# Performance work log

Measured on AMD Instinct MI355X. Metric: run time of the kernel, lower is better.

Reference implementation:

```python
import jax, jax.numpy as jnp
import numpy as np

A, B, I, H, O = 400, 64, 50, 192, 3   # num_agents, batch, input_dim, hidden_dim, output_dim
ADIM, NH = 128, 8                      # attention_dim, num_heads
HD = ADIM // NH
SCALE = HD ** -0.5
EPS = 1e-5


def _ln(x, g, b):
    mu = jnp.mean(x, -1, keepdims=True)
    v = jnp.mean((x - mu) ** 2, -1, keepdims=True)
    return (x - mu) * jax.lax.rsqrt(v + EPS) * g + b


def setup_inputs() -> dict:
    key = jax.random.key(0)
    ks = jax.random.split(key, 12)
    s = 0.05
    n = lambda k, shape: (jax.random.normal(k, shape, jnp.float32) * s)
    return {
        'x': jax.random.normal(ks[0], (B, I), jnp.float32),
        'ln_in_g': jnp.ones((A, I), jnp.float32), 'ln_in_b': jnp.zeros((A, I), jnp.float32),
        'W1': n(ks[1], (A, I, H)), 'b1': jnp.zeros((A, H), jnp.float32),
        'Ws1': n(ks[2], (A, I, H)), 'bs1': jnp.zeros((A, H), jnp.float32),
        'W2': n(ks[3], (A, H, H)), 'b2': jnp.zeros((A, H), jnp.float32),
        'Ws2': n(ks[4], (A, H, H)), 'bs2': jnp.zeros((A, H), jnp.float32),
        'W3': n(ks[5], (A, H, H)), 'b3': jnp.zeros((A, H), jnp.float32),
        'ln_h_g': jnp.ones((A, H), jnp.float32), 'ln_h_b': jnp.zeros((A, H), jnp.float32),
        'Wout': n(ks[6], (A, H, O)), 'bout': jnp.zeros((A, O), jnp.float32),
        'aln_g': jnp.ones((H,), jnp.float32), 'aln_b': jnp.zeros((H,), jnp.float32),
        'Wq': n(ks[7], (H, ADIM)), 'bq': jnp.zeros((ADIM,), jnp.float32),
        'Wk': n(ks[8], (H, ADIM)), 'bk': jnp.zeros((ADIM,), jnp.float32),
        'Wv': n(ks[9], (H, ADIM)), 'bv': jnp.zeros((ADIM,), jnp.float32),
        'Wo': n(ks[10], (ADIM, H)), 'bo': jnp.zeros((H,), jnp.float32),
    }


def _forward(x, ln_in_g, ln_in_b, W1, b1, Ws1, bs1, W2, b2, Ws2, bs2, W3, b3,
             ln_h_g, ln_h_b, Wout, bout, aln_g, aln_b, Wq, bq, Wk, bk, Wv, bv, Wo, bo):
    gelu = lambda t: jax.nn.gelu(t, approximate=False)  # torch F.gelu default = exact erf
    # per-agent input LayerNorm (shared stats, per-agent affine) -> [A, B, I]
    xn = _ln(x[None, :, :], ln_in_g[:, None, :], ln_in_b[:, None, :])
    # agent MLPs as batched GEMMs over agent axis
    h1 = gelu(jnp.einsum('abi,aih->abh', xn, W1) + b1[:, None, :]) \
         + jnp.einsum('abi,aih->abh', xn, Ws1) + bs1[:, None, :]
    h2 = gelu(jnp.einsum('abh,ahk->abk', h1, W2) + b2[:, None, :]) \
         + jnp.einsum('abh,ahk->abk', h1, Ws2) + bs2[:, None, :]
    h3 = _ln(h2 + jnp.einsum('abh,ahk->abk', h2, W3) + b3[:, None, :],
             ln_h_g[:, None, :], ln_h_b[:, None, :])  # [A, B, H]
    # cross-SREK attention across the agent axis
    y = _ln(h3, aln_g, aln_b)
    q = (y @ Wq + bq).reshape(A, B, NH, HD).transpose(1, 2, 0, 3)  # [B, NH, A, HD]
    k = (y @ Wk + bk).reshape(A, B, NH, HD).transpose(1, 2, 0, 3)
    v = (y @ Wv + bv).reshape(A, B, NH, HD).transpose(1, 2, 0, 3)
    attn = jax.nn.softmax(jnp.einsum('bhad,bhcd->bhac', q, k) * SCALE, axis=-1)
    o = jnp.einsum('bhac,bhcd->bhad', attn, v).transpose(2, 0, 1, 3).reshape(A, B, ADIM)
    attended = h3 + (o @ Wo + bo)  # residual (dropout off in eval)
    # per-agent output heads -> [A, B, O]
    logits = jnp.einsum('abh,aho->abo', attended, Wout) + bout[:, None, :]
    return logits


def reference(x, ln_in_g, ln_in_b, W1, b1, Ws1, bs1, W2, b2, Ws2, bs2, W3, b3,
              ln_h_g, ln_h_b, Wout, bout, aln_g, aln_b, Wq, bq, Wk, bk, Wv, bv, Wo, bo):
    return _forward(x, ln_in_g, ln_in_b, W1, b1, Ws1, bs1, W2, b2, Ws2, bs2, W3, b3,
                    ln_h_g, ln_h_b, Wout, bout, aln_g, aln_b, Wq, bq, Wk, bk, Wv, bv, Wo, bo)
```

## Files before the change

### kernel.cpp

```cpp
#include <hip/hip_runtime.h>
#include <math.h>

#define AGENTS 400
#define BATCH  64
#define IDIM   50
#define HDIM   192
#define ODIM   3
#define ADIMM  128
#define NHEADS 8
#define HEADD  16
#define LN_EPS 1e-5f

#define PA   200
#define PAM  192
#define POUT 136

typedef __bf16 bf16x8 __attribute__((ext_vector_type(8)));
typedef float  f32x4  __attribute__((ext_vector_type(4)));

__device__ __forceinline__ float gelu_exact(float x) {
    return 0.5f * x * (1.0f + erff(x * 0.70710678118654752f));
}

__device__ __forceinline__ unsigned pack_bf16x2(float a, float b) {
    unsigned short ua = __builtin_bit_cast(unsigned short, (__bf16)a);
    unsigned short ub = __builtin_bit_cast(unsigned short, (__bf16)b);
    return (unsigned)ua | ((unsigned)ub << 16);
}

__device__ __forceinline__ int as_swz(int row, int col) {
    return ((((col >> 3) ^ (row & 7)) << 3) | (col & 7));
}
__device__ __forceinline__ void st_as(__bf16* As_, int row, int col, float v) {
    As_[row * PAM + as_swz(row, col)] = (__bf16)v;
}
__device__ __forceinline__ float ld_as(const __bf16* As_, int row, int col) {
    return (float)As_[row * PAM + as_swz(row, col)];
}
__device__ __forceinline__ bf16x8 ld_afrag(const __bf16* As_, int row, int k0) {
    int blk = (((k0 >> 3) ^ (row & 7)) << 3);
    return *(const bf16x8*)&As_[row * PAM + blk];
}

#define VMWAIT0()   do { asm volatile("s_waitcnt vmcnt(0)" ::: "memory"); \
                         __builtin_amdgcn_sched_barrier(0); } while (0)
#define BARRIER()   do { __builtin_amdgcn_s_barrier(); \
                         __builtin_amdgcn_sched_barrier(0); } while (0)

struct WPtrs { const float *W1, *Ws1, *W2, *Ws2, *W3; };

__device__ __forceinline__ void issue_slot(int s, float* buf0, float* buf1,
                                           const WPtrs& P, const int* kloc,
                                           const int* nsw, int tid)
{
    const float* M; int c, kdm1;
    if (s < 4)       { M = (s & 1) ? P.Ws1 : P.W1; c = s >> 1;      kdm1 = IDIM - 1; }
    else if (s < 16) { int u = s - 4; M = (u & 1) ? P.Ws2 : P.W2; c = u >> 1; kdm1 = HDIM - 1; }
    else             { M = P.W3; c = s - 16; kdm1 = HDIM - 1; }
    float* dst = (s & 1) ? buf1 : buf0;
    #pragma unroll
    for (int i = 0; i < 6; i++) {
        int kg = c * 32 + kloc[i];
        kg = (kg <= kdm1) ? kg : kdm1;
        const float* src = M + (size_t)kg * HDIM + nsw[i];
        __builtin_amdgcn_global_load_lds(
            (const __attribute__((address_space(1))) void*)src,
            (__attribute__((address_space(3))) void*)(dst + (i * 256 + tid) * 4),
            16, 0, 0);
    }
    __builtin_amdgcn_sched_barrier(0);
}

__device__ __forceinline__ void slot_mfma_f32(f32x4 (&acc)[4][3], const __bf16* As_,
                                              const float* Wbuf, int c, int n0, int lane)
{
    const int r = lane & 15, g = lane >> 4;
    bf16x8 bf[3];
    #pragma unroll
    for (int t = 0; t < 3; t++) {
        int cs = (n0 + 16 * t + r) ^ (g << 3);
        #pragma unroll
        for (int j = 0; j < 8; j++)
            bf[t][j] = (__bf16)Wbuf[(g * 8 + j) * HDIM + cs];
    }
    #pragma unroll
    for (int rg = 0; rg < 4; rg++) {
        bf16x8 af = ld_afrag(As_, 16 * rg + r, c * 32 + g * 8);
        #pragma unroll
        for (int t = 0; t < 3; t++)
            acc[rg][t] = __builtin_amdgcn_mfma_f32_16x16x32_bf16(af, bf[t], acc[rg][t], 0, 0, 0);
    }
}

__global__ __launch_bounds__(256, 2) void mlp_kernel(
    const float* __restrict__ x,
    const float* __restrict__ ln_in_g, const float* __restrict__ ln_in_b,
    const float* __restrict__ W1, const float* __restrict__ b1,
    const float* __restrict__ Ws1, const float* __restrict__ bs1,
    const float* __restrict__ W2, const float* __restrict__ b2,
    const float* __restrict__ Ws2, const float* __restrict__ bs2,
    const float* __restrict__ W3, const float* __restrict__ b3,
    const float* __restrict__ ln_h_g, const float* __restrict__ ln_h_b,
    const float* __restrict__ aln_g, const float* __restrict__ aln_b,
    const float* __restrict__ Wq, const float* __restrict__ bq,
    const float* __restrict__ Wk, const float* __restrict__ bk,
    const float* __restrict__ Wv, const float* __restrict__ bv,
    float* __restrict__ h3out,
    float* __restrict__ qT, float* __restrict__ kT, float* __restrict__ vT)
{
    const int a    = blockIdx.x;
    const int tid  = threadIdx.x;
    const int wave = tid >> 6, lane = tid & 63;
    const int r = lane & 15, g = lane >> 4;
    const int n0 = 48 * wave;

    __shared__ __align__(16) __bf16 As[64 * PAM];
    __shared__ __align__(16) float  Wbuf[2][32 * HDIM];
    __shared__ float mu_s[64], rs_s[64];

    int kloc[6], nsw[6];
    #pragma unroll
    for (int i = 0; i < 6; i++) {
        int w = i * 1024 + tid * 4;
        kloc[i] = w / HDIM;
        int np = w - kloc[i] * HDIM;
        nsw[i] = np ^ (((kloc[i] >> 3) & 3) << 3);
    }

    const WPtrs P = {
        W1  + (size_t)a * IDIM * HDIM,
        Ws1 + (size_t)a * IDIM * HDIM,
        W2  + (size_t)a * HDIM * HDIM,
        Ws2 + (size_t)a * HDIM * HDIM,
        W3  + (size_t)a * HDIM * HDIM };

    {
        int rr = tid >> 2, l = tid & 3;
        float s = 0.f, ss = 0.f;
        for (int k = l; k < IDIM; k += 4) { float v = x[rr * IDIM + k]; s += v; ss += v * v; }
        s  += __shfl_down(s, 2, 4);  s  += __shfl_down(s, 1, 4);
        ss += __shfl_down(ss, 2, 4); ss += __shfl_down(ss, 1, 4);
        if (l == 0) {
            float mu = s * (1.0f / IDIM);
            float var = ss * (1.0f / IDIM) - mu * mu;
            mu_s[rr] = mu;
            rs_s[rr] = rsqrtf(var + LN_EPS);
        }
    }
    __syncthreads();

    issue_slot(0, Wbuf[0], Wbuf[1], P, kloc, nsw, tid);

    for (int sidx = tid; sidx < 64 * 64; sidx += 256) {
        int rr = sidx >> 6, k = sidx & 63;
        float v = 0.f;
        if (k < IDIM)
            v = (x[rr * IDIM + k] - mu_s[rr]) * rs_s[rr] * ln_in_g[a * IDIM + k] + ln_in_b[a * IDIM + k];
        st_as(As, rr, k, v);
    }
    __syncthreads();

    {
        f32x4 acc1[4][3], acc2[4][3];
        #pragma unroll
        for (int i = 0; i < 4; i++)
            #pragma unroll
            for (int t = 0; t < 3; t++) { acc1[i][t] = (f32x4)0.f; acc2[i][t] = (f32x4)0.f; }
        #pragma unroll
        for (int s = 0; s < 4; s++) {
            if (s < 3) issue_slot(s + 1, Wbuf[0], Wbuf[1], P, kloc, nsw, tid);
            if ((s & 1) == 0) slot_mfma_f32(acc1, As, Wbuf[s & 1], s >> 1, n0, lane);
            else              slot_mfma_f32(acc2, As, Wbuf[s & 1], s >> 1, n0, lane);
            VMWAIT0();
            BARRIER();
        }
        issue_slot(4, Wbuf[0], Wbuf[1], P, kloc, nsw, tid);
        #pragma unroll
        for (int t = 0; t < 3; t++) {
            int col = n0 + 16 * t + r;
            float bb  = b1[a * HDIM + col];
            float bbs = bs1[a * HDIM + col];
            #pragma unroll
            for (int rg = 0; rg < 4; rg++)
                #pragma unroll
                for (int i = 0; i < 4; i++) {
                    int row = 16 * rg + 4 * g + i;
                    st_as(As, row, col, gelu_exact(acc1[rg][t][i] + bb) + acc2[rg][t][i] + bbs);
                }
        }
        __syncthreads();
    }

    {
        f32x4 acc1[4][3], acc2[4][3];
        #pragma unroll
        for (int i = 0; i < 4; i++)
            #pragma unroll
            for (int t = 0; t < 3; t++) { acc1[i][t] = (f32x4)0.f; acc2[i][t] = (f32x4)0.f; }
        #pragma unroll
        for (int s = 4; s < 16; s++) {
            if (s < 15) issue_slot(s + 1, Wbuf[0], Wbuf[1], P, kloc, nsw, tid);
            if ((s & 1) == 0) slot_mfma_f32(acc1, As, Wbuf[s & 1], (s - 4) >> 1, n0, lane);
            else              slot_mfma_f32(acc2, As, Wbuf[s & 1], (s - 4) >> 1, n0, lane);
            VMWAIT0();
            BARRIER();
        }
        issue_slot(16, Wbuf[0], Wbuf[1], P, kloc, nsw, tid);
        #pragma unroll
        for (int t = 0; t < 3; t++) {
            int col = n0 + 16 * t + r;
            float bb  = b2[a * HDIM + col];
            float bbs = bs2[a * HDIM + col];
            #pragma unroll
            for (int rg = 0; rg < 4; rg++)
                #pragma unroll
                for (int i = 0; i < 4; i++) {
                    int row = 16 * rg + 4 * g + i;
                    st_as(As, row, col, gelu_exact(acc1[rg][t][i] + bb) + acc2[rg][t][i] + bbs);
                }
        }
        __syncthreads();
    }

    {
        f32x4 acc[4][3];
        #pragma unroll
        for (int i = 0; i < 4; i++)
            #pragma unroll
            for (int t = 0; t < 3; t++) acc[i][t] = (f32x4)0.f;
        #pragma unroll
        for (int s = 16; s < 22; s++) {
            if (s < 21) issue_slot(s + 1, Wbuf[0], Wbuf[1], P, kloc, nsw, tid);
            slot_mfma_f32(acc, As, Wbuf[s & 1], s - 16, n0, lane);
            VMWAIT0();
            BARRIER();
        }
        #pragma unroll
        for (int t = 0; t < 3; t++) {
            int col = n0 + 16 * t + r;
            float bb = b3[a * HDIM + col];
            #pragma unroll
            for (int rg = 0; rg < 4; rg++)
                #pragma unroll
                for (int i = 0; i < 4; i++) {
                    int row = 16 * rg + 4 * g + i;
                    st_as(As, row, col, ld_as(As, row, col) + acc[rg][t][i] + bb);
                }
        }
        __syncthreads();
    }

    {
        int rr = tid >> 2, l = tid & 3;
        float s = 0.f, ss = 0.f;
        for (int k = l; k < HDIM; k += 4) { float v = ld_as(As, rr, k); s += v; ss += v * v; }
        s  += __shfl_down(s, 2, 4);  s  += __shfl_down(s, 1, 4);
        ss += __shfl_down(ss, 2, 4); ss += __shfl_down(ss, 1, 4);
        if (l == 0) {
            float mu = s * (1.0f / HDIM);
            float var = ss * (1.0f / HDIM) - mu * mu;
            mu_s[rr] = mu;
            rs_s[rr] = rsqrtf(var + LN_EPS);
        }
    }
    __syncthreads();
    for (int sidx = tid; sidx < 64 * 48; sidx += 256) {
        int rr = sidx / 48, q = sidx - rr * 48;
        int c = q * 4;
        __bf16* p = &As[rr * PAM + as_swz(rr, c)];
        float4 gv = *(const float4*)&ln_h_g[a * HDIM + c];
        float4 bv = *(const float4*)&ln_h_b[a * HDIM + c];
        float mu = mu_s[rr], rs = rs_s[rr];
        float4 o;
        o.x = ((float)p[0] - mu) * rs * gv.x + bv.x;
        o.y = ((float)p[1] - mu) * rs * gv.y + bv.y;
        o.z = ((float)p[2] - mu) * rs * gv.z + bv.z;
        o.w = ((float)p[3] - mu) * rs * gv.w + bv.w;
        *(float4*)&h3out[((size_t)a * BATCH + rr) * HDIM + c] = o;
        p[0] = (__bf16)o.x; p[1] = (__bf16)o.y; p[2] = (__bf16)o.z; p[3] = (__bf16)o.w;
    }
    __syncthreads();

    {
        int rr = tid >> 2, l = tid & 3;
        float s = 0.f, ss = 0.f;
        for (int k = l; k < HDIM; k += 4) { float v = ld_as(As, rr, k); s += v; ss += v * v; }
        s  += __shfl_down(s, 2, 4);  s  += __shfl_down(s, 1, 4);
        ss += __shfl_down(ss, 2, 4); ss += __shfl_down(ss, 1, 4);
        if (l == 0) {
            float mu = s * (1.0f / HDIM);
            float var = ss * (1.0f / HDIM) - mu * mu;
            mu_s[rr] = mu;
            rs_s[rr] = rsqrtf(var + LN_EPS);
        }
    }
    __syncthreads();
    for (int sidx = tid; sidx < 64 * HDIM; sidx += 256) {
        int rr = sidx / HDIM, c = sidx - rr * HDIM;
        float v = (ld_as(As, rr, c) - mu_s[rr]) * rs_s[rr] * aln_g[c] + aln_b[c];
        st_as(As, rr, c, v);
    }
    __syncthreads();

    #pragma unroll
    for (int p = 0; p < 2; p++) {
        const int nb = 192 * p + 48 * wave;
        const float* wA[3];
        #pragma unroll
        for (int t = 0; t < 3; t++) {
            int nt = nb + 16 * t;
            const float* base = (nt < 128) ? Wq : (nt < 256) ? Wk : Wv;
            wA[t] = base + (nt & 127);
        }
        f32x4 acc[4][3];
        #pragma unroll
        for (int i = 0; i < 4; i++)
            #pragma unroll
            for (int t = 0; t < 3; t++) acc[i][t] = (f32x4)0.f;

        float buf[2][24];
        #pragma unroll
        for (int t = 0; t < 3; t++)
            #pragma unroll
            for (int j = 0; j < 8; j++)
                buf[0][t * 8 + j] = wA[t][(g * 8 + j) * ADIMM + r];
        #pragma unroll
        for (int c = 0; c < 6; c++) {
            const int cur = c & 1, nxt = cur ^ 1;
            if (c < 5) {
                #pragma unroll
                for (int t = 0; t < 3; t++)
                    #pragma unroll
                    for (int j = 0; j < 8; j++)
                        buf[nxt][t * 8 + j] = wA[t][((c + 1) * 32 + g * 8 + j) * ADIMM + r];
            }
            bf16x8 bfr[3];
            #pragma unroll
            for (int t = 0; t < 3; t++)
                #pragma unroll
                for (int j = 0; j < 8; j++)
                    bfr[t][j] = (__bf16)buf[cur][t * 8 + j];
            #pragma unroll
            for (int rg = 0; rg < 4; rg++) {
                bf16x8 af = ld_afrag(As, 16 * rg + r, c * 32 + g * 8);
                #pragma unroll
                for (int t = 0; t < 3; t++)
                    acc[rg][t] = __builtin_amdgcn_mfma_f32_16x16x32_bf16(af, bfr[t], acc[rg][t], 0, 0, 0);
            }
        }

        #pragma unroll
        for (int t = 0; t < 3; t++) {
            int n = nb + 16 * t + r;
            int which = n >> 7, cc = n & 127, hh = cc >> 4, dd = cc & 15;
            const float* bp = (which == 0) ? bq : (which == 1) ? bk : bv;
            float* op = (which == 0) ? qT : (which == 1) ? kT : vT;
            float bb = bp[cc];
            #pragma unroll
            for (int rg = 0; rg < 4; rg++)
                #pragma unroll
                for (int i = 0; i < 4; i++) {
                    int brow = 16 * rg + 4 * g + i;
                    op[(((size_t)brow * NHEADS + hh) * AGENTS + a) * HEADD + dd] = acc[rg][t][i] + bb;
                }
        }
    }
}

template<int NC, int KD, int NT, int NRG, int LDW, int PITCH>
__device__ __forceinline__ void gemm_bpass(f32x4 (&acc)[NRG][NT],
                                           const float* const* wptr,
                                           const __bf16* Asrc, int lane)
{
    const int r = lane & 15, g = lane >> 4;
    float buf[2][NT * 8];

    #pragma unroll
    for (int t = 0; t < NT; t++)
        #pragma unroll
        for (int j = 0; j < 8; j++) {
            int k = g * 8 + j;
            buf[0][t * 8 + j] = (k < KD) ? wptr[t][k * LDW + r] : 0.f;
        }

    #pragma unroll
    for (int c = 0; c < NC; c++) {
        const int cur = c & 1, nxt = cur ^ 1;
        if (c + 1 < NC) {
            #pragma unroll
            for (int t = 0; t < NT; t++)
                #pragma unroll
                for (int j = 0; j < 8; j++) {
                    int k = (c + 1) * 32 + g * 8 + j;
                    buf[nxt][t * 8 + j] = (k < KD) ? wptr[t][k * LDW + r] : 0.f;
                }
        }
        bf16x8 bfr[NT];
        #pragma unroll
        for (int t = 0; t < NT; t++)
            #pragma unroll
            for (int j = 0; j < 8; j++)
                bfr[t][j] = (__bf16)buf[cur][t * 8 + j];
        #pragma unroll
        for (int rg = 0; rg < NRG; rg++) {
            bf16x8 af = *(const bf16x8*)&Asrc[(16 * rg + r) * PITCH + c * 32 + g * 8];
            #pragma unroll
            for (int t = 0; t < NT; t++)
                acc[rg][t] = __builtin_amdgcn_mfma_f32_16x16x32_bf16(af, bfr[t], acc[rg][t], 0, 0, 0);
        }
    }
}

#define PKA 24
#define PVA 408
#define PPA 232

__global__ __launch_bounds__(256, 2) void attn_kernel(
    const float* __restrict__ qT, const float* __restrict__ kT,
    const float* __restrict__ vT, float* __restrict__ oT)
{
    const int bh   = blockIdx.x;
    const int b    = bh >> 3, h = bh & 7;
    const int tid  = threadIdx.x;
    const int wave = tid >> 6, lane = tid & 63;
    const int r = lane & 15, g = lane >> 4;

    __shared__ __align__(16) __bf16 Ks[AGENTS * PKA];
    __shared__ __align__(16) __bf16 Vt[16 * PVA];
    __shared__ __align__(16) __bf16 Ps[4][16 * PPA];

    const float* kp = kT + (size_t)bh * AGENTS * HEADD;
    const float* vp = vT + (size_t)bh * AGENTS * HEADD;
    for (int idx4 = tid; idx4 < AGENTS * HEADD / 4; idx4 += 256) {
        int a_ = idx4 >> 2, d0 = (idx4 & 3) << 2;
        float4 kv = *(const float4*)(kp + a_ * HEADD + d0);
        float4 vv = *(const float4*)(vp + a_ * HEADD + d0);
        *(uint2*)&Ks[a_ * PKA + d0] =
            make_uint2(pack_bf16x2(kv.x, kv.y), pack_bf16x2(kv.z, kv.w));
        Vt[(d0 + 0) * PVA + a_] = (__bf16)vv.x;
        Vt[(d0 + 1) * PVA + a_] = (__bf16)vv.y;
        Vt[(d0 + 2) * PVA + a_] = (__bf16)vv.z;
        Vt[(d0 + 3) * PVA + a_] = (__bf16)vv.w;
    }
    __bf16* Pw = Ps[wave];
    for (int z = lane; z < 16 * 16; z += 64)
        Pw[(z >> 4) * PPA + 208 + (z & 15)] = (__bf16)0.f;
    __syncthreads();

    float qf[8];
    auto loadq = [&](int mt_) {
        if (g < 2) {
            const float* qp = qT + ((size_t)bh * AGENTS + mt_ * 16 + r) * HEADD + g * 8;
            float4 v0 = *(const float4*)qp;
            float4 v1 = *(const float4*)(qp + 4);
            qf[0] = v0.x; qf[1] = v0.y; qf[2] = v0.z; qf[3] = v0.w;
            qf[4] = v1.x; qf[5] = v1.y; qf[6] = v1.z; qf[7] = v1.w;
        }
    };
    loadq(wave);

    for (int mt = wave; mt < 25; mt += 4) {
        const int m0 = mt * 16;

        bf16x8 aq;
        #pragma unroll
        for (int j = 0; j < 8; j++)
            aq[j] = (g < 2) ? (__bf16)(qf[j] * 0.25f) : (__bf16)0.f;

        f32x4 sacc[25];
        #pragma unroll
        for (int t = 0; t < 25; t++) {
            bf16x8 bk_ = *(const bf16x8*)&Ks[(t * 16 + r) * PKA + (g & 1) * 8];
            sacc[t] = __builtin_amdgcn_mfma_f32_16x16x32_bf16(aq, bk_, (f32x4)0.f, 0, 0, 0);
        }

        if (mt + 4 < 25) loadq(mt + 4);

        float lv[4];
        #pragma unroll
        for (int i = 0; i < 4; i++) {
            float tm[16];
            #pragma unroll
            for (int t = 0; t < 9; t++) tm[t] = fmaxf(sacc[t][i], sacc[t + 16][i]);
            #pragma unroll
            for (int t = 9; t < 16; t++) tm[t] = sacc[t][i];
            #pragma unroll
            for (int off = 8; off; off >>= 1)
                #pragma unroll
                for (int t = 0; t < off; t++) tm[t] = fmaxf(tm[t], tm[t + off]);
            float m_ = tm[0];
            #pragma unroll
            for (int off = 8; off; off >>= 1) m_ = fmaxf(m_, __shfl_xor(m_, off, 16));

            #pragma unroll
            for (int t = 0; t < 25; t++) sacc[t][i] = __expf(sacc[t][i] - m_);

            float ts[16];
            #pragma unroll
            for (int t = 0; t < 9; t++) ts[t] = sacc[t][i] + sacc[t + 16][i];
            #pragma unroll
            for (int t = 9; t < 16; t++) ts[t] = sacc[t][i];
            #pragma unroll
            for (int off = 8; off; off >>= 1)
                #pragma unroll
                for (int t = 0; t < off; t++) ts[t] += ts[t + off];
            float l_ = ts[0];
            #pragma unroll
            for (int off = 8; off; off >>= 1) l_ += __shfl_xor(l_, off, 16);
            lv[i] = l_;
        }

        f32x4 oacc = (f32x4)0.f;

        #pragma unroll
        for (int t = 0; t < 13; t++)
            #pragma unroll
            for (int i = 0; i < 4; i++)
                Pw[(g * 4 + i) * PPA + t * 16 + r] = (__bf16)sacc[t][i];
        __asm__ volatile("s_waitcnt lgkmcnt(0)" ::: "memory");
        #pragma unroll
        for (int c = 0; c < 7; c++) {
            bf16x8 ap  = *(const bf16x8*)&Pw[r * PPA + c * 32 + g * 8];
            bf16x8 bv_ = *(const bf16x8*)&Vt[r * PVA + c * 32 + g * 8];
            oacc = __builtin_amdgcn_mfma_f32_16x16x32_bf16(ap, bv_, oacc, 0, 0, 0);
        }

        #pragma unroll
        for (int t = 13; t < 25; t++)
            #pragma unroll
            for (int i = 0; i < 4; i++)
                Pw[(g * 4 + i) * PPA + (t - 13) * 16 + r] = (__bf16)sacc[t][i];
        __asm__ volatile("s_waitcnt lgkmcnt(0)" ::: "memory");
        #pragma unroll
        for (int c = 0; c < 6; c++) {
            bf16x8 ap  = *(const bf16x8*)&Pw[r * PPA + c * 32 + g * 8];
            bf16x8 bv_ = *(const bf16x8*)&Vt[r * PVA + 208 + c * 32 + g * 8];
            oacc = __builtin_amdgcn_mfma_f32_16x16x32_bf16(ap, bv_, oacc, 0, 0, 0);
        }

        #pragma unroll
        for (int i = 0; i < 4; i++) {
            float rl = __builtin_amdgcn_rcpf(lv[i]);
            oT[((size_t)(m0 + g * 4 + i) * BATCH + b) * ADIMM + h * HEADD + r] = oacc[i] * rl;
        }
    }
}

__global__ __launch_bounds__(256, 2) void out_kernel(
    const float* __restrict__ h3, const float* __restrict__ oT,
    const float* __restrict__ Wo, const float* __restrict__ bo,
    const float* __restrict__ Wout, const float* __restrict__ bout,
    float* __restrict__ out)
{
    const int a    = blockIdx.x;
    const int tid  = threadIdx.x;
    const int wave = tid >> 6, lane = tid & 63;
    const int r = lane & 15, g = lane >> 4;
    const int n0 = 48 * wave;

    __shared__ __align__(16) __bf16 os[64 * POUT];
    __shared__ __align__(16) __bf16 att[64 * PA];
    __shared__ __align__(16) float  wout_s[HDIM * ODIM];

    float h3v[3][4][4];
    #pragma unroll
    for (int t = 0; t < 3; t++) {
        int col = n0 + 16 * t + r;
        #pragma unroll
        for (int rg = 0; rg < 4; rg++)
            #pragma unroll
            for (int i = 0; i < 4; i++)
                h3v[t][rg][i] = h3[((size_t)a * BATCH + 16 * rg + 4 * g + i) * HDIM + col];
    }

    for (int idx = tid; idx < 64 * 32; idx += 256) {
        int bb = idx >> 5, q = idx & 31;
        float4 v = ((const float4*)(oT + ((size_t)a * BATCH + bb) * ADIMM))[q];
        unsigned u0 = pack_bf16x2(v.x, v.y);
        unsigned u1 = pack_bf16x2(v.z, v.w);
        *(uint2*)&os[bb * POUT + q * 4] = make_uint2(u0, u1);
    }
    {
        const float4* src = (const float4*)(Wout + (size_t)a * HDIM * ODIM);
        for (int idx = tid; idx < HDIM * ODIM / 4; idx += 256)
            ((float4*)wout_s)[idx] = src[idx];
    }
    __syncthreads();

    {
        const float* wA[3] = { Wo + n0, Wo + n0 + 16, Wo + n0 + 32 };
        f32x4 acc[4][3];
        #pragma unroll
        for (int i = 0; i < 4; i++)
            #pragma unroll
            for (int t = 0; t < 3; t++) acc[i][t] = (f32x4)0.f;
        gemm_bpass<4, ADIMM, 3, 4, HDIM, POUT>(acc, wA, os, lane);
        #pragma unroll
        for (int t = 0; t < 3; t++) {
            int col = n0 + 16 * t + r;
            float bb = bo[col];
            #pragma unroll
            for (int rg = 0; rg < 4; rg++)
                #pragma unroll
                for (int i = 0; i < 4; i++) {
                    int row = 16 * rg + 4 * g + i;
                    float v = h3v[t][rg][i] + acc[rg][t][i] + bb;
                    att[row * PA + col] = (__bf16)v;
                }
        }
    }
    __syncthreads();

    {
        float wb[48];
        #pragma unroll
        for (int c = 0; c < 6; c++)
            #pragma unroll
            for (int j = 0; j < 8; j++) {
                int k = c * 32 + g * 8 + j;
                wb[c * 8 + j] = (r < ODIM) ? wout_s[k * ODIM + r] : 0.f;
            }
        f32x4 oacc = (f32x4)0.f;
        #pragma unroll
        for (int c = 0; c < 6; c++) {
            bf16x8 bf;
            #pragma unroll
            for (int j = 0; j < 8; j++) bf[j] = (__bf16)wb[c * 8 + j];
            bf16x8 af = *(const bf16x8*)&att[(16 * wave + r) * PA + c * 32 + g * 8];
            oacc = __builtin_amdgcn_mfma_f32_16x16x32_bf16(af, bf, oacc, 0, 0, 0);
        }
        if (r < ODIM) {
            float bb = bout[a * ODIM + r];
            #pragma unroll
            for (int i = 0; i < 4; i++) {
                int row = 16 * wave + 4 * g + i;
                out[((size_t)a * BATCH + row) * ODIM + r] = oacc[i] + bb;
            }
        }
    }
}

extern "C" void kernel_launch(void* const* d_in, const int* in_sizes, int n_in,
                              void* d_out, int out_size, void* d_ws, size_t ws_size,
                              hipStream_t stream)
{
    const float* x       = (const float*)d_in[0];
    const float* ln_in_g = (const float*)d_in[1];
    const float* ln_in_b = (const float*)d_in[2];
    const float* W1      = (const float*)d_in[3];
    const float* b1      = (const float*)d_in[4];
    const float* Ws1     = (const float*)d_in[5];
    const float* bs1     = (const float*)d_in[6];
    const float* W2      = (const float*)d_in[7];
    const float* b2      = (const float*)d_in[8];
    const float* Ws2     = (const float*)d_in[9];
    const float* bs2     = (const float*)d_in[10];
    const float* W3      = (const float*)d_in[11];
    const float* b3      = (const float*)d_in[12];
    const float* ln_h_g  = (const float*)d_in[13];
    const float* ln_h_b  = (const float*)d_in[14];
    const float* Wout    = (const float*)d_in[15];
    const float* bout    = (const float*)d_in[16];
    const float* aln_g   = (const float*)d_in[17];
    const float* aln_b   = (const float*)d_in[18];
    const float* Wq      = (const float*)d_in[19];
    const float* bq      = (const float*)d_in[20];
    const float* Wk      = (const float*)d_in[21];
    const float* bk      = (const float*)d_in[22];
    const float* Wv      = (const float*)d_in[23];
    const float* bv      = (const float*)d_in[24];
    const float* Wo      = (const float*)d_in[25];
    const float* bo      = (const float*)d_in[26];
    float* out = (float*)d_out;

    float* ws = (float*)d_ws;
    const size_t H3_SZ = (size_t)AGENTS * BATCH * HDIM;
    const size_t QT_SZ = (size_t)BATCH * NHEADS * AGENTS * HEADD;
    float* h3 = ws;
    float* qT = h3 + H3_SZ;
    float* kT = qT + QT_SZ;
    float* vT = kT + QT_SZ;
    float* oT = vT + QT_SZ;

    mlp_kernel<<<AGENTS, 256, 0, stream>>>(x, ln_in_g, ln_in_b,
                                           W1, b1, Ws1, bs1, W2, b2, Ws2, bs2,
                                           W3, b3, ln_h_g, ln_h_b,
                                           aln_g, aln_b, Wq, bq, Wk, bk, Wv, bv,
                                           h3, qT, kT, vT);
    attn_kernel<<<BATCH * NHEADS, 256, 0, stream>>>(qT, kT, vT, oT);
    out_kernel<<<AGENTS, 256, 0, stream>>>(h3, oT, Wo, bo, Wout, bout, out);
}
```

Baseline: 356.8 us.

## Stage MLP weights through registers into bf16 LDS instead of direct global-to-LDS

The MLP kernel's weight streaming changes from direct global_load_lds of fp32 tiles to loads into registers. Each thread then converts the values to bf16 and writes a swizzled bf16 tile into LDS. This halves the LDS footprint of the weight double buffer and removes the per-element fp32-to-bf16 conversion in the MFMA fragment loads. The cost is an extra barrier per slot and register pressure from holding the prefetched float4s. The attention kernel's K tile pitch is also changed from 24 to 44, likely to alter LDS bank mapping.

```diff
diff --git a/kernel.cpp b/kernel.cpp
--- a/kernel.cpp
+++ b/kernel.cpp
@@ -49,39 +49,51 @@
 
 struct WPtrs { const float *W1, *Ws1, *W2, *Ws2, *W3; };
 
-__device__ __forceinline__ void issue_slot(int s, float* buf0, float* buf1,
-                                           const WPtrs& P, const int* kloc,
-                                           const int* nsw, int tid)
-{
-    const float* M; int c, kdm1;
+__device__ __forceinline__ void slot_src(int s, const WPtrs& P,
+                                         const float*& M, int& c, int& kdm1)
+{
     if (s < 4)       { M = (s & 1) ? P.Ws1 : P.W1; c = s >> 1;      kdm1 = IDIM - 1; }
     else if (s < 16) { int u = s - 4; M = (u & 1) ? P.Ws2 : P.W2; c = u >> 1; kdm1 = HDIM - 1; }
     else             { M = P.W3; c = s - 16; kdm1 = HDIM - 1; }
-    float* dst = (s & 1) ? buf1 : buf0;
+}
+
+__device__ __forceinline__ void issue_loads(int s, float4 (&G)[6], const WPtrs& P,
+                                            const int* kloc, const int* npl)
+{
+    const float* M; int c, kdm1;
+    slot_src(s, P, M, c, kdm1);
     #pragma unroll
     for (int i = 0; i < 6; i++) {
         int kg = c * 32 + kloc[i];
         kg = (kg <= kdm1) ? kg : kdm1;
-        const float* src = M + (size_t)kg * HDIM + nsw[i];
-        __builtin_amdgcn_global_load_lds(
-            (const __attribute__((address_space(1))) void*)src,
-            (__attribute__((address_space(3))) void*)(dst + (i * 256 + tid) * 4),
-            16, 0, 0);
-    }
-    __builtin_amdgcn_sched_barrier(0);
-}
-
-__device__ __forceinline__ void slot_mfma_f32(f32x4 (&acc)[4][3], const __bf16* As_,
-                                              const float* Wbuf, int c, int n0, int lane)
+        G[i] = *(const float4*)(M + (size_t)kg * HDIM + npl[i]);
+    }
+}
+
+__device__ __forceinline__ void write_slot(float4 (&G)[6], __bf16* buf,
+                                           const int* kloc, const int* npl)
+{
+    #pragma unroll
+    for (int i = 0; i < 6; i++) {
+        int k = kloc[i];
+        int npe = npl[i] ^ (((k >> 3) & 3) << 3);
+        unsigned u0 = pack_bf16x2(G[i].x, G[i].y);
+        unsigned u1 = pack_bf16x2(G[i].z, G[i].w);
+        *(uint2*)&buf[k * HDIM + npe] = make_uint2(u0, u1);
+    }
+}
+
+__device__ __forceinline__ void slot_mfma_bf(f32x4 (&acc)[4][3], const __bf16* As_,
+                                             const __bf16* Wb, int c, int n0, int lane)
 {
     const int r = lane & 15, g = lane >> 4;
     bf16x8 bf[3];
     #pragma unroll
     for (int t = 0; t < 3; t++) {
-        int cs = (n0 + 16 * t + r) ^ (g << 3);
+        int csx = (n0 + 16 * t + r) ^ (g << 3);
         #pragma unroll
         for (int j = 0; j < 8; j++)
-            bf[t][j] = (__bf16)Wbuf[(g * 8 + j) * HDIM + cs];
+            bf[t][j] = Wb[(g * 8 + j) * HDIM + csx];
     }
     #pragma unroll
     for (int rg = 0; rg < 4; rg++) {
@@ -115,16 +127,15 @@
     const int n0 = 48 * wave;
 
     __shared__ __align__(16) __bf16 As[64 * PAM];
-    __shared__ __align__(16) float  Wbuf[2][32 * HDIM];
+    __shared__ __align__(16) __bf16 Wb[2][32 * HDIM];
     __shared__ float mu_s[64], rs_s[64];
 
-    int kloc[6], nsw[6];
+    int kloc[6], npl[6];
     #pragma unroll
     for (int i = 0; i < 6; i++) {
         int w = i * 1024 + tid * 4;
         kloc[i] = w / HDIM;
-        int np = w - kloc[i] * HDIM;
-        nsw[i] = np ^ (((kloc[i] >> 3) & 3) << 3);
+        npl[i]  = w - kloc[i] * HDIM;
     }
 
     const WPtrs P = {
@@ -133,6 +144,8 @@
         W2  + (size_t)a * HDIM * HDIM,
         Ws2 + (size_t)a * HDIM * HDIM,
         W3  + (size_t)a * HDIM * HDIM };
+
+    float4 G[6];
 
     {
         int rr = tid >> 2, l = tid & 3;
@@ -149,7 +162,7 @@
     }
     __syncthreads();
 
-    issue_slot(0, Wbuf[0], Wbuf[1], P, kloc, nsw, tid);
+    issue_loads(0, G, P, kloc, npl);
 
     for (int sidx = tid; sidx < 64 * 64; sidx += 256) {
         int rr = sidx >> 6, k = sidx & 63;
@@ -158,6 +171,8 @@
             v = (x[rr * IDIM + k] - mu_s[rr]) * rs_s[rr] * ln_in_g[a * IDIM + k] + ln_in_b[a * IDIM + k];
         st_as(As, rr, k, v);
     }
+    VMWAIT0();
+    write_slot(G, Wb[0], kloc, npl);
     __syncthreads();
 
     {
@@ -168,13 +183,14 @@
             for (int t = 0; t < 3; t++) { acc1[i][t] = (f32x4)0.f; acc2[i][t] = (f32x4)0.f; }
         #pragma unroll
         for (int s = 0; s < 4; s++) {
-            if (s < 3) issue_slot(s + 1, Wbuf[0], Wbuf[1], P, kloc, nsw, tid);
-            if ((s & 1) == 0) slot_mfma_f32(acc1, As, Wbuf[s & 1], s >> 1, n0, lane);
-            else              slot_mfma_f32(acc2, As, Wbuf[s & 1], s >> 1, n0, lane);
+            issue_loads(s + 1, G, P, kloc, npl);
+            if ((s & 1) == 0) slot_mfma_bf(acc1, As, Wb[s & 1], s >> 1, n0, lane);
+            else              slot_mfma_bf(acc2, As, Wb[s & 1], s >> 1, n0, lane);
+            BARRIER();
             VMWAIT0();
-            BARRIER();
-        }
-        issue_slot(4, Wbuf[0], Wbuf[1], P, kloc, nsw, tid);
+            write_slot(G, Wb[(s + 1) & 1], kloc, npl);
+            __syncthreads();
+        }
         #pragma unroll
         for (int t = 0; t < 3; t++) {
             int col = n0 + 16 * t + r;
@@ -199,13 +215,14 @@
             for (int t = 0; t < 3; t++) { acc1[i][t] = (f32x4)0.f; acc2[i][t] = (f32x4)0.f; }
         #pragma unroll
         for (int s = 4; s < 16; s++) {
-            if (s < 15) issue_slot(s + 1, Wbuf[0], Wbuf[1], P, kloc, nsw, tid);
-            if ((s & 1) == 0) slot_mfma_f32(acc1, As, Wbuf[s & 1], (s - 4) >> 1, n0, lane);
-            else              slot_mfma_f32(acc2, As, Wbuf[s & 1], (s - 4) >> 1, n0, lane);
+            issue_loads(s + 1, G, P, kloc, npl);
+            if ((s & 1) == 0) slot_mfma_bf(acc1, As, Wb[s & 1], (s - 4) >> 1, n0, lane);
+            else              slot_mfma_bf(acc2, As, Wb[s & 1], (s - 4) >> 1, n0, lane);
+            BARRIER();
             VMWAIT0();
-            BARRIER();
-        }
-        issue_slot(16, Wbuf[0], Wbuf[1], P, kloc, nsw, tid);
+            write_slot(G, Wb[(s + 1) & 1], kloc, npl);
+            __syncthreads();
+        }
         #pragma unroll
         for (int t = 0; t < 3; t++) {
             int col = n0 + 16 * t + r;
@@ -230,10 +247,14 @@
             for (int t = 0; t < 3; t++) acc[i][t] = (f32x4)0.f;
         #pragma unroll
         for (int s = 16; s < 22; s++) {
-            if (s < 21) issue_slot(s + 1, Wbuf[0], Wbuf[1], P, kloc, nsw, tid);
-            slot_mfma_f32(acc, As, Wbuf[s & 1], s - 16, n0, lane);
-            VMWAIT0();
+            if (s < 21) issue_loads(s + 1, G, P, kloc, npl);
+            slot_mfma_bf(acc, As, Wb[s & 1], s - 16, n0, lane);
             BARRIER();
+            if (s < 21) {
+                VMWAIT0();
+                write_slot(G, Wb[(s + 1) & 1], kloc, npl);
+            }
+            __syncthreads();
         }
         #pragma unroll
         for (int t = 0; t < 3; t++) {
@@ -411,7 +432,7 @@
     }
 }
 
-#define PKA 24
+#define PKA 44
 #define PVA 408
 #define PPA 232
 
```

Result: slower. 376.8 us (+5.6%).

## Split MLP kernel batch rows across two blocks per agent

Applied to the files above, without the earlier changes.

The MLP kernel now launches two blocks per agent, each handling 32 of the 64 batch rows, instead of one block covering all 64. The intent is to use more of the MI355X's compute units (400 blocks underfill the device), and the smaller per-block accumulator and LDS footprint should also help occupancy. In exchange, every agent's weights are streamed twice, once by each block, which doubles weight traffic from global memory or L2 and halves MFMA reuse per loaded weight tile.

```diff
diff --git a/kernel.cpp b/kernel.cpp
--- a/kernel.cpp
+++ b/kernel.cpp
@@ -14,6 +14,7 @@
 #define PA   200
 #define PAM  192
 #define POUT 136
+#define MROWS 32
 
 typedef __bf16 bf16x8 __attribute__((ext_vector_type(8)));
 typedef float  f32x4  __attribute__((ext_vector_type(4)));
@@ -71,7 +72,7 @@
     __builtin_amdgcn_sched_barrier(0);
 }
 
-__device__ __forceinline__ void slot_mfma_f32(f32x4 (&acc)[4][3], const __bf16* As_,
+__device__ __forceinline__ void slot_mfma_f32(f32x4 (&acc)[2][3], const __bf16* As_,
                                               const float* Wbuf, int c, int n0, int lane)
 {
     const int r = lane & 15, g = lane >> 4;
@@ -84,7 +85,7 @@
             bf[t][j] = (__bf16)Wbuf[(g * 8 + j) * HDIM + cs];
     }
     #pragma unroll
-    for (int rg = 0; rg < 4; rg++) {
+    for (int rg = 0; rg < 2; rg++) {
         bf16x8 af = ld_afrag(As_, 16 * rg + r, c * 32 + g * 8);
         #pragma unroll
         for (int t = 0; t < 3; t++)
@@ -108,15 +109,17 @@
     float* __restrict__ h3out,
     float* __restrict__ qT, float* __restrict__ kT, float* __restrict__ vT)
 {
-    const int a    = blockIdx.x;
+    const int bid  = blockIdx.x;
+    const int a    = bid % AGENTS;
+    const int rb   = (bid / AGENTS) * MROWS;
     const int tid  = threadIdx.x;
     const int wave = tid >> 6, lane = tid & 63;
     const int r = lane & 15, g = lane >> 4;
     const int n0 = 48 * wave;
 
-    __shared__ __align__(16) __bf16 As[64 * PAM];
+    __shared__ __align__(16) __bf16 As[MROWS * PAM];
     __shared__ __align__(16) float  Wbuf[2][32 * HDIM];
-    __shared__ float mu_s[64], rs_s[64];
+    __shared__ float mu_s[MROWS], rs_s[MROWS];
 
     int kloc[6], nsw[6];
     #pragma unroll
@@ -135,11 +138,12 @@
         W3  + (size_t)a * HDIM * HDIM };
 
     {
-        int rr = tid >> 2, l = tid & 3;
+        int rr = tid >> 3, l = tid & 7;
+        const float* xp = x + (size_t)(rb + rr) * IDIM;
         float s = 0.f, ss = 0.f;
-        for (int k = l; k < IDIM; k += 4) { float v = x[rr * IDIM + k]; s += v; ss += v * v; }
-        s  += __shfl_down(s, 2, 4);  s  += __shfl_down(s, 1, 4);
-        ss += __shfl_down(ss, 2, 4); ss += __shfl_down(ss, 1, 4);
+        for (int k = l; k < IDIM; k += 8) { float v = xp[k]; s += v; ss += v * v; }
+        s  += __shfl_down(s, 4, 8); s  += __shfl_down(s, 2, 8); s  += __shfl_down(s, 1, 8);
+        ss += __shfl_down(ss, 4, 8); ss += __shfl_down(ss, 2, 8); ss += __shfl_down(ss, 1, 8);
         if (l == 0) {
             float mu = s * (1.0f / IDIM);
             float var = ss * (1.0f / IDIM) - mu * mu;
@@ -151,19 +155,20 @@
 
     issue_slot(0, Wbuf[0], Wbuf[1], P, kloc, nsw, tid);
 
-    for (int sidx = tid; sidx < 64 * 64; sidx += 256) {
+    for (int sidx = tid; sidx < MROWS * 64; sidx += 256) {
         int rr = sidx >> 6, k = sidx & 63;
         float v = 0.f;
         if (k < IDIM)
-            v = (x[rr * IDIM + k] - mu_s[rr]) * rs_s[rr] * ln_in_g[a * IDIM + k] + ln_in_b[a * IDIM + k];
+            v = (x[(size_t)(rb + rr) * IDIM + k] - mu_s[rr]) * rs_s[rr]
+                * ln_in_g[a * IDIM + k] + ln_in_b[a * IDIM + k];
         st_as(As, rr, k, v);
     }
     __syncthreads();
 
     {
-        f32x4 acc1[4][3], acc2[4][3];
-        #pragma unroll
-        for (int i = 0; i < 4; i++)
+        f32x4 acc1[2][3], acc2[2][3];
+        #pragma unroll
+        for (int i = 0; i < 2; i++)
             #pragma unroll
             for (int t = 0; t < 3; t++) { acc1[i][t] = (f32x4)0.f; acc2[i][t] = (f32x4)0.f; }
         #pragma unroll
@@ -181,7 +186,7 @@
             float bb  = b1[a * HDIM + col];
             float bbs = bs1[a * HDIM + col];
             #pragma unroll
-            for (int rg = 0; rg < 4; rg++)
+            for (int rg = 0; rg < 2; rg++)
                 #pragma unroll
                 for (int i = 0; i < 4; i++) {
                     int row = 16 * rg + 4 * g + i;
@@ -192,9 +197,9 @@
     }
 
     {
-        f32x4 acc1[4][3], acc2[4][3];
-        #pragma unroll
-        for (int i = 0; i < 4; i++)
+        f32x4 acc1[2][3], acc2[2][3];
+        #pragma unroll
+        for (int i = 0; i < 2; i++)
             #pragma unroll
             for (int t = 0; t < 3; t++) { acc1[i][t] = (f32x4)0.f; acc2[i][t] = (f32x4)0.f; }
         #pragma unroll
@@ -212,7 +217,7 @@
             float bb  = b2[a * HDIM + col];
             float bbs = bs2[a * HDIM + col];
             #pragma unroll
-            for (int rg = 0; rg < 4; rg++)
+            for (int rg = 0; rg < 2; rg++)
                 #pragma unroll
                 for (int i = 0; i < 4; i++) {
                     int row = 16 * rg + 4 * g + i;
@@ -223,9 +228,9 @@
     }
 
     {
-        f32x4 acc[4][3];
-        #pragma unroll
-        for (int i = 0; i < 4; i++)
+        f32x4 acc[2][3];
+        #pragma unroll
+        for (int i = 0; i < 2; i++)
             #pragma unroll
             for (int t = 0; t < 3; t++) acc[i][t] = (f32x4)0.f;
         #pragma unroll
@@ -240,7 +245,7 @@
             int col = n0 + 16 * t + r;
             float bb = b3[a * HDIM + col];
             #pragma unroll
-            for (int rg = 0; rg < 4; rg++)
+            for (int rg = 0; rg < 2; rg++)
                 #pragma unroll
                 for (int i = 0; i < 4; i++) {
                     int row = 16 * rg + 4 * g + i;
@@ -251,11 +256,11 @@
     }
 
     {
-        int rr = tid >> 2, l = tid & 3;
+        int rr = tid >> 3, l = tid & 7;
         float s = 0.f, ss = 0.f;
-        for (int k = l; k < HDIM; k += 4) { float v = ld_as(As, rr, k); s += v; ss += v * v; }
-        s  += __shfl_down(s, 2, 4);  s  += __shfl_down(s, 1, 4);
-        ss += __shfl_down(ss, 2, 4); ss += __shfl_down(ss, 1, 4);
+        for (int k = l; k < HDIM; k += 8) { float v = ld_as(As, rr, k); s += v; ss += v * v; }
+        s  += __shfl_down(s, 4, 8); s  += __shfl_down(s, 2, 8); s  += __shfl_down(s, 1, 8);
+        ss += __shfl_down(ss, 4, 8); ss += __shfl_down(ss, 2, 8); ss += __shfl_down(ss, 1, 8);
         if (l == 0) {
             float mu = s * (1.0f / HDIM);
             float var = ss * (1.0f / HDIM) - mu * mu;
@@ -264,7 +269,7 @@
         }
     }
     __syncthreads();
-    for (int sidx = tid; sidx < 64 * 48; sidx += 256) {
+    for (int sidx = tid; sidx < MROWS * 48; sidx += 256) {
         int rr = sidx / 48, q = sidx - rr * 48;
         int c = q * 4;
         __bf16* p = &As[rr * PAM + as_swz(rr, c)];
@@ -276,17 +281,17 @@
         o.y = ((float)p[1] - mu) * rs * gv.y + bv.y;
         o.z = ((float)p[2] - mu) * rs * gv.z + bv.z;
         o.w = ((float)p[3] - mu) * rs * gv.w + bv.w;
-        *(float4*)&h3out[((size_t)a * BATCH + rr) * HDIM + c] = o;
+        *(float4*)&h3out[((size_t)a * BATCH + rb + rr) * HDIM + c] = o;
         p[0] = (__bf16)o.x; p[1] = (__bf16)o.y; p[2] = (__bf16)o.z; p[3] = (__bf16)o.w;
     }
     __syncthreads();
 
     {
-        int rr = tid >> 2, l = tid & 3;
+        int rr = tid >> 3, l = tid & 7;
         float s = 0.f, ss = 0.f;
-        for (int k = l; k < HDIM; k += 4) { float v = ld_as(As, rr, k); s += v; ss += v * v; }
-        s  += __shfl_down(s, 2, 4);  s  += __shfl_down(s, 1, 4);
-        ss += __shfl_down(ss, 2, 4); ss += __shfl_down(ss, 1, 4);
+        for (int k = l; k < HDIM; k += 8) { float v = ld_as(As, rr, k); s += v; ss += v * v; }
+        s  += __shfl_down(s, 4, 8); s  += __shfl_down(s, 2, 8); s  += __shfl_down(s, 1, 8);
+        ss += __shfl_down(ss, 4, 8); ss += __shfl_down(ss, 2, 8); ss += __shfl_down(ss, 1, 8);
         if (l == 0) {
             float mu = s * (1.0f / HDIM);
             float var = ss * (1.0f / HDIM) - mu * mu;
@@ -295,7 +300,7 @@
         }
     }
     __syncthreads();
-    for (int sidx = tid; sidx < 64 * HDIM; sidx += 256) {
+    for (int sidx = tid; sidx < MROWS * HDIM; sidx += 256) {
         int rr = sidx / HDIM, c = sidx - rr * HDIM;
         float v = (ld_as(As, rr, c) - mu_s[rr]) * rs_s[rr] * aln_g[c] + aln_b[c];
         st_as(As, rr, c, v);
@@ -312,9 +317,9 @@
             const float* base = (nt < 128) ? Wq : (nt < 256) ? Wk : Wv;
             wA[t] = base + (nt & 127);
         }
-        f32x4 acc[4][3];
-        #pragma unroll
-        for (int i = 0; i < 4; i++)
+        f32x4 acc[2][3];
+        #pragma unroll
+        for (int i = 0; i < 2; i++)
             #pragma unroll
             for (int t = 0; t < 3; t++) acc[i][t] = (f32x4)0.f;
 
@@ -341,7 +346,7 @@
                 for (int j = 0; j < 8; j++)
                     bfr[t][j] = (__bf16)buf[cur][t * 8 + j];
             #pragma unroll
-            for (int rg = 0; rg < 4; rg++) {
+            for (int rg = 0; rg < 2; rg++) {
                 bf16x8 af = ld_afrag(As, 16 * rg + r, c * 32 + g * 8);
                 #pragma unroll
                 for (int t = 0; t < 3; t++)
@@ -357,10 +362,10 @@
             float* op = (which == 0) ? qT : (which == 1) ? kT : vT;
             float bb = bp[cc];
             #pragma unroll
-            for (int rg = 0; rg < 4; rg++)
+            for (int rg = 0; rg < 2; rg++)
                 #pragma unroll
                 for (int i = 0; i < 4; i++) {
-                    int brow = 16 * rg + 4 * g + i;
+                    int brow = rb + 16 * rg + 4 * g + i;
                     op[(((size_t)brow * NHEADS + hh) * AGENTS + a) * HEADD + dd] = acc[rg][t][i] + bb;
                 }
         }
@@ -682,11 +687,11 @@
     float* vT = kT + QT_SZ;
     float* oT = vT + QT_SZ;
 
-    mlp_kernel<<<AGENTS, 256, 0, stream>>>(x, ln_in_g, ln_in_b,
-                                           W1, b1, Ws1, bs1, W2, b2, Ws2, bs2,
-                                           W3, b3, ln_h_g, ln_h_b,
-                                           aln_g, aln_b, Wq, bq, Wk, bk, Wv, bv,
-                                           h3, qT, kT, vT);
+    mlp_kernel<<<AGENTS * 2, 256, 0, stream>>>(x, ln_in_g, ln_in_b,
+                                               W1, b1, Ws1, bs1, W2, b2, Ws2, bs2,
+                                               W3, b3, ln_h_g, ln_h_b,
+                                               aln_g, aln_b, Wq, bq, Wk, bk, Wv, bv,
+                                               h3, qT, kT, vT);
     attn_kernel<<<BATCH * NHEADS, 256, 0, stream>>>(qT, kT, vT, oT);
     out_kernel<<<AGENTS, 256, 0, stream>>>(h3, oT, Wo, bo, Wout, bout, out);
 }
```

Result: slower. 364.3 us (+2.1%).
